# Performance work log

Measured on AMD Instinct MI355X. Metric: run time of the kernel, lower is better.

Reference implementation:

```python
import jax, jax.numpy as jnp
import numpy as np
import math

D_MODEL = 512
NHEAD = 8
HEAD_DIM = D_MODEL // NHEAD
MAX_REL = 128
B, T, S = 4, 2048, 2048


def setup_inputs() -> dict:
    key = jax.random.key(0)
    ks = jax.random.split(key, 16)
    sc = 1.0 / math.sqrt(D_MODEL)
    inp = {
        "query": jax.random.normal(ks[0], (B, T, D_MODEL), jnp.float32),
        "key": jax.random.normal(ks[1], (B, S, D_MODEL), jnp.float32),
        "value": jax.random.normal(ks[2], (B, S, D_MODEL), jnp.float32),
        "Wq": jax.random.normal(ks[3], (D_MODEL, D_MODEL), jnp.float32) * sc,
        "bq": jnp.zeros((D_MODEL,), jnp.float32),
        "Wk": jax.random.normal(ks[4], (D_MODEL, D_MODEL), jnp.float32) * sc,
        "bk": jnp.zeros((D_MODEL,), jnp.float32),
        "Wv": jax.random.normal(ks[5], (D_MODEL, D_MODEL), jnp.float32) * sc,
        "bv": jnp.zeros((D_MODEL,), jnp.float32),
        "Wo": jax.random.normal(ks[6], (D_MODEL, D_MODEL), jnp.float32) * sc,
        "bo": jnp.zeros((D_MODEL,), jnp.float32),
        "rel_emb": jax.random.normal(ks[7], (2 * MAX_REL + 1, NHEAD), jnp.float32) * 0.02,
    }
    return inp


def reference(query, key, value, Wq, bq, Wk, bk, Wv, bv, Wo, bo, rel_emb):
    # linear projections (torch Linear: x @ W.T + b), split heads -> [B,H,T,Dh]
    def proj(x, W, b, L):
        return (x @ W.T + b).reshape(B, L, NHEAD, HEAD_DIM).transpose(0, 2, 1, 3)

    q = proj(query, Wq, bq, T)
    k = proj(key, Wk, bk, S)
    v = proj(value, Wv, bv, S)

    scores = jnp.einsum("bhtd,bhsd->bhts", q, k) / math.sqrt(HEAD_DIM)

    # relative position bias lookup: rel[t,s] = clamp(t-s) + max_rel -> [H,T,S]
    rel = jnp.arange(T)[:, None] - jnp.arange(S)[None, :]
    rel = jnp.clip(rel, -MAX_REL, MAX_REL) + MAX_REL
    bias = rel_emb[rel].transpose(2, 0, 1)  # [H,T,S]
    scores = scores + bias[None]

    w = jax.nn.softmax(scores, axis=-1)  # dropout p used in eval mode -> identity
    out = jnp.einsum("bhts,bhsd->bhtd", w, v)
    out = out.transpose(0, 2, 1, 3).reshape(B, T, D_MODEL)
    return out @ Wo.T + bo
```

## Files before the change

### kernel.cpp

```cpp
#include <hip/hip_runtime.h>

typedef __attribute__((ext_vector_type(4))) float f32x4;
typedef __attribute__((ext_vector_type(16))) float f32x16;
typedef __attribute__((ext_vector_type(4))) unsigned short u16x4;
typedef __attribute__((ext_vector_type(8))) unsigned short u16x8;
typedef __attribute__((ext_vector_type(4))) unsigned int u32x4;
typedef __attribute__((ext_vector_type(8))) __bf16 bf16x8;

#define SZX_E ((size_t)4 * 2048 * 512)
#define SZW_E ((size_t)512 * 512)

__device__ __forceinline__ unsigned short f2bf(float f) {
  unsigned int u = __builtin_bit_cast(unsigned int, f);
  u += 0x7fffu + ((u >> 16) & 1u);
  return (unsigned short)(u >> 16);
}

__device__ __forceinline__ bf16x8 ld_bf8(const unsigned short* p) {
  return __builtin_bit_cast(bf16x8, *(const u16x8*)p);
}

__device__ __forceinline__ f32x4 mfma16(bf16x8 a, bf16x8 b, f32x4 c) {
  return __builtin_amdgcn_mfma_f32_16x16x32_bf16(a, b, c, 0, 0, 0);
}

__device__ __forceinline__ f32x16 mfma32(bf16x8 a, bf16x8 b, f32x16 c) {
  return __builtin_amdgcn_mfma_f32_32x32x16_bf16(a, b, c, 0, 0, 0);
}

__device__ __forceinline__ unsigned int cvt_pk_bf16(float lo, float hi) {
  unsigned int r;
  asm("v_cvt_pk_bf16_f32 %0, %1, %2" : "=v"(r) : "v"(lo), "v"(hi));
  return r;
}

__device__ __forceinline__ void plane32_swap(unsigned int& a, unsigned int& b) {
  asm("v_permlane32_swap_b32 %0, %1" : "+v"(a), "+v"(b));
}

__device__ __forceinline__ float exp2_fast(float x) {
  float r;
  asm("v_exp_f32 %0, %1" : "=v"(r) : "v"(x));
  return r;
}

__device__ __forceinline__ void gload16(const void* g, void* l) {
  __builtin_amdgcn_global_load_lds(
      (const __attribute__((address_space(1))) unsigned int*)g,
      (__attribute__((address_space(3))) unsigned int*)l, 16, 0, 0);
}

__global__ __launch_bounds__(256) void cvt_all(const float* __restrict__ q_,
                                               const float* __restrict__ k_,
                                               const float* __restrict__ v_,
                                               const float* __restrict__ wq_,
                                               const float* __restrict__ wk_,
                                               const float* __restrict__ wv_,
                                               const float* __restrict__ wo_,
                                               unsigned short* __restrict__ out) {
  const int bq = blockIdx.x;
  const float* src;
  size_t segbase, li;
  if (bq < 12288) {
    const int s = bq >> 12;
    src = (s == 0) ? q_ : (s == 1) ? k_ : v_;
    li = (size_t)(bq & 4095) * 256 + threadIdx.x;
    segbase = (size_t)s * 4194304;
  } else {
    const int s = (bq - 12288) >> 8;
    src = (s == 0) ? wq_ : (s == 1) ? wk_ : (s == 2) ? wv_ : wo_;
    li = (size_t)((bq - 12288) & 255) * 256 + threadIdx.x;
    segbase = 12582912 + (size_t)s * 262144;
  }
  const f32x4 v = *(const f32x4*)(src + li * 4);
  u16x4 r;
  r[0] = f2bf(v[0]); r[1] = f2bf(v[1]); r[2] = f2bf(v[2]); r[3] = f2bf(v[3]);
  *(u16x4*)(out + segbase + li * 4) = r;
}

__global__ __launch_bounds__(256) void gemm_qkv(const unsigned short* __restrict__ base,
                                                const float* __restrict__ bq,
                                                const float* __restrict__ bk,
                                                const float* __restrict__ bv,
                                                unsigned short* __restrict__ outb) {
  __shared__ unsigned short Asb[2][4096];
  __shared__ unsigned short Bsb[2][4096];
  const int z = blockIdx.z;
  const unsigned short* A = base + (size_t)z * SZX_E;
  const unsigned short* Bw = base + 3 * SZX_E + (size_t)z * SZW_E;
  const float* bias = (z == 0) ? bq : (z == 1) ? bk : bv;

  const int tid = threadIdx.x;
  const int l = tid & 63;
  const int w = tid >> 6;
  const int g = l >> 4;
  const int lr = l & 15;
  const int mB = blockIdx.y * 128;
  const int nB = blockIdx.x * 128;
  const int m0 = (w >> 1) * 64;
  const int n0 = (w & 1) * 64;
  const int ubase = tid & ~63;

  auto stage = [&](int bufi, int kk) {
#pragma unroll
    for (int i = 0; i < 2; i++) {
      const int idx = i * 256 + tid;
      const int ub = i * 256 + ubase;
      const int r = idx >> 2, c = idx & 3;
      gload16((const char*)A + ((size_t)(mB + r) * 512 + kk + c * 8) * 2,
              (char*)&Asb[bufi][0] + ub * 16);
      gload16((const char*)Bw + ((size_t)(nB + r) * 512 + kk + c * 8) * 2,
              (char*)&Bsb[bufi][0] + ub * 16);
    }
  };

  f32x4 acc[4][4];
#pragma unroll
  for (int i = 0; i < 4; i++)
#pragma unroll
    for (int j = 0; j < 4; j++) acc[i][j] = f32x4{0.f, 0.f, 0.f, 0.f};

  stage(0, 0);
  __syncthreads();
  int buf = 0;

  for (int ks = 0; ks < 16; ++ks) {
    if (ks < 15) stage(buf ^ 1, (ks + 1) * 32);
    bf16x8 af[4], bfr[4];
#pragma unroll
    for (int t = 0; t < 4; t++) {
      af[t] = ld_bf8(&Asb[buf][(m0 + t * 16 + lr) * 32 + g * 8]);
      bfr[t] = ld_bf8(&Bsb[buf][(n0 + t * 16 + lr) * 32 + g * 8]);
    }
#pragma unroll
    for (int i = 0; i < 4; i++)
#pragma unroll
      for (int j = 0; j < 4; j++)
        acc[i][j] = mfma16(af[i], bfr[j], acc[i][j]);
    __syncthreads();
    buf ^= 1;
  }

  unsigned short* outz = outb + (size_t)z * SZX_E;
#pragma unroll
  for (int j = 0; j < 4; j++) {
    const int n = nB + n0 + j * 16 + lr;
    const float bn = bias[n];
#pragma unroll
    for (int i = 0; i < 4; i++) {
#pragma unroll
      for (int r = 0; r < 4; r++) {
        const int m = mB + m0 + i * 16 + g * 4 + r;
        const float v = acc[i][j][r] + bn;
        if (z < 2) {
          outz[(size_t)m * 512 + n] = f2bf(v);
        } else {
          const int bb = m >> 11, s = m & 2047;
          const int hh = n >> 6, d = n & 63;
          outz[((size_t)((bb * 8 + hh) * 64 + d) << 11) + s] = f2bf(v);
        }
      }
    }
  }
}

__global__ __launch_bounds__(256) void gemm_o(const unsigned short* __restrict__ A,
                                              const unsigned short* __restrict__ Bw,
                                              const float* __restrict__ bias,
                                              float* __restrict__ Cout) {
  __shared__ unsigned short Asb[2][4096];
  __shared__ unsigned short Bsb[2][4096];
  const int tid = threadIdx.x;
  const int l = tid & 63;
  const int w = tid >> 6;
  const int g = l >> 4;
  const int lr = l & 15;
  const int mB = blockIdx.y * 128;
  const int nB = blockIdx.x * 128;
  const int m0 = (w >> 1) * 64;
  const int n0 = (w & 1) * 64;
  const int ubase = tid & ~63;

  auto stage = [&](int bufi, int kk) {
#pragma unroll
    for (int i = 0; i < 2; i++) {
      const int idx = i * 256 + tid;
      const int ub = i * 256 + ubase;
      const int r = idx >> 2, c = idx & 3;
      gload16((const char*)A + ((size_t)(mB + r) * 512 + kk + c * 8) * 2,
              (char*)&Asb[bufi][0] + ub * 16);
      gload16((const char*)Bw + ((size_t)(nB + r) * 512 + kk + c * 8) * 2,
              (char*)&Bsb[bufi][0] + ub * 16);
    }
  };

  f32x4 acc[4][4];
#pragma unroll
  for (int i = 0; i < 4; i++)
#pragma unroll
    for (int j = 0; j < 4; j++) acc[i][j] = f32x4{0.f, 0.f, 0.f, 0.f};

  stage(0, 0);
  __syncthreads();
  int buf = 0;

  for (int ks = 0; ks < 16; ++ks) {
    if (ks < 15) stage(buf ^ 1, (ks + 1) * 32);
    bf16x8 af[4], bfr[4];
#pragma unroll
    for (int t = 0; t < 4; t++) {
      af[t] = ld_bf8(&Asb[buf][(m0 + t * 16 + lr) * 32 + g * 8]);
      bfr[t] = ld_bf8(&Bsb[buf][(n0 + t * 16 + lr) * 32 + g * 8]);
    }
#pragma unroll
    for (int i = 0; i < 4; i++)
#pragma unroll
      for (int j = 0; j < 4; j++)
        acc[i][j] = mfma16(af[i], bfr[j], acc[i][j]);
    __syncthreads();
    buf ^= 1;
  }

#pragma unroll
  for (int j = 0; j < 4; j++) {
    const int n = nB + n0 + j * 16 + lr;
    const float bn = bias[n];
#pragma unroll
    for (int i = 0; i < 4; i++) {
#pragma unroll
      for (int r = 0; r < 4; r++) {
        const int m = mB + m0 + i * 16 + g * 4 + r;
        Cout[(size_t)m * 512 + n] = acc[i][j][r] + bn;
      }
    }
  }
}

__global__ __launch_bounds__(256, 2) void attn_kernel(const unsigned short* __restrict__ Qp,
                                                      const unsigned short* __restrict__ Kp,
                                                      const unsigned short* __restrict__ Vt,
                                                      const float* __restrict__ rel_emb,
                                                      unsigned short* __restrict__ At) {
  __shared__ float bias_s[257];
  __shared__ unsigned short K_lds[2][4096];
  __shared__ unsigned short V_lds[2][4096];
  const int bid0 = blockIdx.x;
  const int lg = (bid0 & 7) * 64 + (bid0 >> 3);
  const int qb = lg & 15;
  const int h = (lg >> 4) & 7;
  const int b = lg >> 7;
  const int tid = threadIdx.x;
  const int lane = tid & 63, w = tid >> 6;
  const int hi = lane >> 5, q31 = lane & 31;
  const int q0w = qb * 128 + w * 32;
  const int tq = q0w + q31;
  const float SCL = 0.125f * 1.44269504f;

  const bool isK = (w < 2);
  const char* sbase = isK ? (const char*)Kp + ((size_t)b * 2048 * 512 + h * 64) * 2
                          : (const char*)Vt + ((size_t)(b * 8 + h) * 64 * 2048) * 2;
  const size_t step = isK ? (size_t)64 * 1024 : 128;
  const int i0 = (w & 1) * 4;
  const int rr0 = (i0 + 0) * 8 + (lane >> 3), ch0 = (lane & 7) ^ (rr0 & 7);
  const int rr1 = (i0 + 1) * 8 + (lane >> 3), ch1 = (lane & 7) ^ (rr1 & 7);
  const int rr2 = (i0 + 2) * 8 + (lane >> 3), ch2 = (lane & 7) ^ (rr2 & 7);
  const int rr3 = (i0 + 3) * 8 + (lane >> 3), ch3 = (lane & 7) ^ (rr3 & 7);
  const size_t rstr = isK ? 1024 : 4096;
  const char* gp0 = sbase + (size_t)rr0 * rstr + ch0 * 16;
  const char* gp1 = sbase + (size_t)rr1 * rstr + ch1 * 16;
  const char* gp2 = sbase + (size_t)rr2 * rstr + ch2 * 16;
  const char* gp3 = sbase + (size_t)rr3 * rstr + ch3 * 16;
  char* db0 = (isK ? (char*)&K_lds[0][0] : (char*)&V_lds[0][0]) + i0 * 4096 / 4;
  char* db1 = (isK ? (char*)&K_lds[1][0] : (char*)&V_lds[1][0]) + i0 * 1024;

  auto STAGE = [&](char* dbase) {
    gload16(gp0, dbase);
    gload16(gp1, dbase + 1024);
    gload16(gp2, dbase + 2048);
    gload16(gp3, dbase + 3072);
    gp0 += step; gp1 += step; gp2 += step; gp3 += step;
  };

  for (int i = tid; i < 257; i += 256) bias_s[i] = rel_emb[i * 8 + h] * 1.44269504f;
  STAGE(db0);
  __syncthreads();
  const float bias_lo = bias_s[0], bias_hi = bias_s[256];

  const unsigned short* qptr = Qp + (size_t)(b * 2048 + tq) * 512 + h * 64 + hi * 8;
  const bf16x8 qf0 = ld_bf8(qptr);
  const bf16x8 qf1 = ld_bf8(qptr + 16);
  const bf16x8 qf2 = ld_bf8(qptr + 32);
  const bf16x8 qf3 = ld_bf8(qptr + 48);

  const int rswz = q31 & 7;
  int koff[4], voff[4];
#pragma unroll
  for (int c = 0; c < 4; c++) koff[c] = q31 * 64 + (((2 * c + hi) ^ rswz) << 3);
#pragma unroll
  for (int ks = 0; ks < 4; ks++) voff[ks] = q31 * 64 + (((ks * 2 + hi) ^ rswz) << 3);

  const f32x16 z16 = {0.f, 0.f, 0.f, 0.f, 0.f, 0.f, 0.f, 0.f,
                      0.f, 0.f, 0.f, 0.f, 0.f, 0.f, 0.f, 0.f};
  f32x16 o_lo = z16, o_hi = z16;
  float l_run = 0.f;

  auto TILE = [&](const unsigned short* kb, const unsigned short* vb, int s0) {
    f32x16 sa, sb;
    sa = mfma32(ld_bf8(kb + koff[0]), qf0, z16);
    sb = mfma32(ld_bf8(kb + 2048 + koff[0]), qf0, z16);
    sa = mfma32(ld_bf8(kb + koff[1]), qf1, sa);
    sb = mfma32(ld_bf8(kb + 2048 + koff[1]), qf1, sb);
    sa = mfma32(ld_bf8(kb + koff[2]), qf2, sa);
    sb = mfma32(ld_bf8(kb + 2048 + koff[2]), qf2, sb);
    sa = mfma32(ld_bf8(kb + koff[3]), qf3, sa);
    sb = mfma32(ld_bf8(kb + 2048 + koff[3]), qf3, sb);

    bf16x8 vl[4], vh[4];
#pragma unroll
    for (int ks = 0; ks < 4; ks++) {
      vl[ks] = ld_bf8(vb + voff[ks]);
      vh[ks] = ld_bf8(vb + 2048 + voff[ks]);
    }

    const int relmin = q0w - s0 - 63;
    const int relmax = q0w + 31 - s0;
    float SCL2, off0;
    if (relmin >= 128 || relmax <= -128) {
      SCL2 = SCL;
      off0 = (relmin >= 128) ? bias_hi : bias_lo;
    } else {
#pragma unroll
      for (int r = 0; r < 16; r++) {
        const int rowA = (r & 3) + 8 * (r >> 2) + 4 * hi;
        const int rA = tq - s0 - rowA;
        const int rB = rA - 32;
        const int iA = (rA < -128 ? -128 : (rA > 128 ? 128 : rA)) + 128;
        const int iB = (rB < -128 ? -128 : (rB > 128 ? 128 : rB)) + 128;
        sa[r] = fmaf(sa[r], SCL, bias_s[iA]);
        sb[r] = fmaf(sb[r], SCL, bias_s[iB]);
      }
      SCL2 = 1.f;
      off0 = 0.f;
    }

#pragma unroll
    for (int r = 0; r < 16; r++) {
      sa[r] = exp2_fast(fmaf(sa[r], SCL2, off0));
      sb[r] = exp2_fast(fmaf(sb[r], SCL2, off0));
    }
    float s8[8];
#pragma unroll
    for (int i = 0; i < 8; i++)
      s8[i] = (sa[i] + sa[i + 8]) + (sb[i] + sb[i + 8]);
    float ps = ((s8[0] + s8[1]) + (s8[2] + s8[3])) + ((s8[4] + s8[5]) + (s8[6] + s8[7]));
    ps += __shfl_xor(ps, 32, 64);
    l_run += ps;

    bf16x8 pa[4];
#pragma unroll
    for (int ks = 0; ks < 4; ks++) {
      const int c8 = (ks & 1) * 8;
      const f32x16& src = (ks < 2) ? sa : sb;
      unsigned int a0 = cvt_pk_bf16(src[c8 + 0], src[c8 + 1]);
      unsigned int b0 = cvt_pk_bf16(src[c8 + 4], src[c8 + 5]);
      unsigned int a1 = cvt_pk_bf16(src[c8 + 2], src[c8 + 3]);
      unsigned int b1 = cvt_pk_bf16(src[c8 + 6], src[c8 + 7]);
      plane32_swap(a0, b0);
      plane32_swap(a1, b1);
      pa[ks] = __builtin_bit_cast(bf16x8, u32x4{a0, a1, b0, b1});
    }

#pragma unroll
    for (int ks = 0; ks < 4; ks++) {
      o_lo = mfma32(pa[ks], vl[ks], o_lo);
      o_hi = mfma32(pa[ks], vh[ks], o_hi);
    }
  };

  const unsigned short* K0 = &K_lds[0][0];
  const unsigned short* K1 = &K_lds[1][0];
  const unsigned short* V0 = &V_lds[0][0];
  const unsigned short* V1 = &V_lds[1][0];

  for (int t = 0; t < 32; t += 2) {
    STAGE(db1);
    TILE(K0, V0, t * 64);
    __syncthreads();
    if (t + 2 < 32) STAGE(db0);
    TILE(K1, V1, (t + 1) * 64);
    __syncthreads();
  }

  const float inv = 1.f / l_run;
#pragma unroll
  for (int r2 = 0; r2 < 16; r2++) {
    const int ro = (r2 & 3) + 8 * (r2 >> 2) + 4 * hi;
    const float rr = __shfl(inv, ro, 64);
    unsigned short* op = At + (size_t)(b * 2048 + q0w + ro) * 512 + h * 64;
    op[q31] = f2bf(o_lo[r2] * rr);
    op[32 + q31] = f2bf(o_hi[r2] * rr);
  }
}

extern "C" void kernel_launch(void* const* d_in, const int* in_sizes, int n_in,
                              void* d_out, int out_size, void* d_ws, size_t ws_size,
                              hipStream_t stream) {
  const float* query = (const float*)d_in[0];
  const float* key   = (const float*)d_in[1];
  const float* value = (const float*)d_in[2];
  const float* Wq = (const float*)d_in[3];
  const float* bq = (const float*)d_in[4];
  const float* Wk = (const float*)d_in[5];
  const float* bk = (const float*)d_in[6];
  const float* Wv = (const float*)d_in[7];
  const float* bv = (const float*)d_in[8];
  const float* Wo = (const float*)d_in[9];
  const float* bo = (const float*)d_in[10];
  const float* rel = (const float*)d_in[11];

  char* ws = (char*)d_ws;
  unsigned short* base = (unsigned short*)ws;
  unsigned short* wo = base + 3 * SZX_E + 3 * SZW_E;
  unsigned short* Qp = base + 3 * SZX_E + 4 * SZW_E;
  unsigned short* Kp = Qp + SZX_E;
  unsigned short* Vt = Kp + SZX_E;
  unsigned short* At = Vt + SZX_E;

  cvt_all<<<dim3(13312), dim3(256), 0, stream>>>(query, key, value, Wq, Wk, Wv, Wo, base);

  dim3 blk(256);
  gemm_qkv<<<dim3(4, 64, 3), blk, 0, stream>>>(base, bq, bk, bv, Qp);

  attn_kernel<<<dim3(512), blk, 0, stream>>>(Qp, Kp, Vt, rel, At);

  gemm_o<<<dim3(4, 64), blk, 0, stream>>>(At, wo, bo, (float*)d_out);
}
```

Baseline: 104.8 us.

## Swizzle GEMM block order and hoist K/V fragment loads ahead of MFMAs

```diff
diff --git a/kernel.cpp b/kernel.cpp
--- a/kernel.cpp
+++ b/kernel.cpp
@@ -95,8 +95,10 @@
   const int w = tid >> 6;
   const int g = l >> 4;
   const int lr = l & 15;
-  const int mB = blockIdx.y * 128;
-  const int nB = blockIdx.x * 128;
+  const int bid = blockIdx.x + (blockIdx.y << 2);
+  const int lgg = (bid & 7) * 32 + (bid >> 3);
+  const int nB = (lgg & 3) * 128;
+  const int mB = (lgg >> 2) * 128;
   const int m0 = (w >> 1) * 64;
   const int n0 = (w & 1) * 64;
   const int ubase = tid & ~63;
@@ -175,8 +177,10 @@
   const int w = tid >> 6;
   const int g = l >> 4;
   const int lr = l & 15;
-  const int mB = blockIdx.y * 128;
-  const int nB = blockIdx.x * 128;
+  const int bid = blockIdx.x + (blockIdx.y << 2);
+  const int lgg = (bid & 7) * 32 + (bid >> 3);
+  const int nB = (lgg & 3) * 128;
+  const int mB = (lgg >> 2) * 128;
   const int m0 = (w >> 1) * 64;
   const int n0 = (w & 1) * 64;
   const int ubase = tid & ~63;
@@ -270,7 +274,7 @@
   const char* gp1 = sbase + (size_t)rr1 * rstr + ch1 * 16;
   const char* gp2 = sbase + (size_t)rr2 * rstr + ch2 * 16;
   const char* gp3 = sbase + (size_t)rr3 * rstr + ch3 * 16;
-  char* db0 = (isK ? (char*)&K_lds[0][0] : (char*)&V_lds[0][0]) + i0 * 4096 / 4;
+  char* db0 = (isK ? (char*)&K_lds[0][0] : (char*)&V_lds[0][0]) + i0 * 1024;
   char* db1 = (isK ? (char*)&K_lds[1][0] : (char*)&V_lds[1][0]) + i0 * 1024;
 
   auto STAGE = [&](char* dbase) {
@@ -305,22 +309,30 @@
   float l_run = 0.f;
 
   auto TILE = [&](const unsigned short* kb, const unsigned short* vb, int s0) {
-    f32x16 sa, sb;
-    sa = mfma32(ld_bf8(kb + koff[0]), qf0, z16);
-    sb = mfma32(ld_bf8(kb + 2048 + koff[0]), qf0, z16);
-    sa = mfma32(ld_bf8(kb + koff[1]), qf1, sa);
-    sb = mfma32(ld_bf8(kb + 2048 + koff[1]), qf1, sb);
-    sa = mfma32(ld_bf8(kb + koff[2]), qf2, sa);
-    sb = mfma32(ld_bf8(kb + 2048 + koff[2]), qf2, sb);
-    sa = mfma32(ld_bf8(kb + koff[3]), qf3, sa);
-    sb = mfma32(ld_bf8(kb + 2048 + koff[3]), qf3, sb);
-
+    bf16x8 kfl0 = ld_bf8(kb + koff[0]);
+    bf16x8 kfh0 = ld_bf8(kb + 2048 + koff[0]);
+    bf16x8 kfl1 = ld_bf8(kb + koff[1]);
+    bf16x8 kfh1 = ld_bf8(kb + 2048 + koff[1]);
+    bf16x8 kfl2 = ld_bf8(kb + koff[2]);
+    bf16x8 kfh2 = ld_bf8(kb + 2048 + koff[2]);
+    bf16x8 kfl3 = ld_bf8(kb + koff[3]);
+    bf16x8 kfh3 = ld_bf8(kb + 2048 + koff[3]);
     bf16x8 vl[4], vh[4];
 #pragma unroll
     for (int ks = 0; ks < 4; ks++) {
       vl[ks] = ld_bf8(vb + voff[ks]);
       vh[ks] = ld_bf8(vb + 2048 + voff[ks]);
     }
+
+    f32x16 sa, sb;
+    sa = mfma32(kfl0, qf0, z16);
+    sb = mfma32(kfh0, qf0, z16);
+    sa = mfma32(kfl1, qf1, sa);
+    sb = mfma32(kfh1, qf1, sb);
+    sa = mfma32(kfl2, qf2, sa);
+    sb = mfma32(kfh2, qf2, sb);
+    sa = mfma32(kfl3, qf3, sa);
+    sb = mfma32(kfh3, qf3, sb);
 
     const int relmin = q0w - s0 - 63;
     const int relmax = q0w + 31 - s0;
```

Result: faster. 102.2 us (-2.5%).
